# Kernel optimization log

Hardware: AMD Instinct MI355X
Metric: run time of the kernel (lower is better)

The kernel has to match this reference:

```python
import jax, jax.numpy as jnp
import numpy as np

B, T, D_IN = 16, 4096, 512
D_EMB, N_CODES = 256, 1024


def setup_inputs() -> dict:
    key = jax.random.key(0)
    k1, k2, k3, k4 = jax.random.split(key, 4)
    z = jax.random.normal(k1, (B, T, D_IN), dtype=jnp.float32)
    embedding = jax.random.normal(k2, (N_CODES, D_EMB), dtype=jnp.float32)
    # torch Linear weight layout [out_features, in_features], bias=False
    proj_down_w = jax.random.normal(k3, (D_EMB, D_IN), dtype=jnp.float32) * (1.0 / np.sqrt(D_IN))
    proj_up_w = jax.random.normal(k4, (D_IN, D_EMB), dtype=jnp.float32) * (1.0 / np.sqrt(D_EMB))
    return {"z": z, "embedding": embedding, "proj_down_w": proj_down_w, "proj_up_w": proj_up_w}


def _quantize_to_code(z_e, codebook):
    # z_e: [b, t, d]; codebook: [n, d] -> indices [b, t]
    b, t, d = z_e.shape
    z_flat = z_e.reshape(b * t, d)
    dist = (jnp.sum(z_flat * z_flat, axis=1, keepdims=True)
            - 2.0 * (z_flat @ codebook.T)
            + jnp.sum(codebook * codebook, axis=1)[None, :])  # [(b t), n]
    return jnp.argmin(dist, axis=1).reshape(b, t)


def reference(z, embedding, proj_down_w, proj_up_w):
    # proj_down: z @ W_down^T
    z_e = jnp.einsum('btd,ed->bte', z, proj_down_w)  # [b, t, D_EMB]
    code = _quantize_to_code(z_e, embedding)
    z_q = embedding[code]  # gather: [b, t, D_EMB]
    diff2 = (z_q - z_e) ** 2
    commitment_loss = diff2.mean(axis=(1, 2))  # [b]
    codebook_loss = diff2.mean(axis=(1, 2))    # [b] (same values fwd; differ in grad)
    # straight-through estimator (training mode)
    z_q_st = z_e + jax.lax.stop_gradient(z_q - z_e)
    z_q_out = jnp.einsum('bte,de->btd', z_q_st, proj_up_w)  # [b, t, D_IN]
    return (z_q_out, commitment_loss, codebook_loss, code, z_e)
```

## Files before the change

kernel.cpp:

```cpp
#include <hip/hip_runtime.h>
#include <stdint.h>

#define DIN  512
#define DE   256
#define NC   1024
#define M_   65536
#define FLAGCAP 16384

typedef unsigned short u16;
typedef __attribute__((ext_vector_type(8))) short short8_t;
typedef __attribute__((ext_vector_type(4))) float f32x4_t;
typedef __attribute__((ext_vector_type(16))) float f32x16_t;

__device__ __forceinline__ float bf2f(u16 u) {
    unsigned x = ((unsigned)u) << 16; return __builtin_bit_cast(float, x);
}
__device__ __forceinline__ u16 f2bf(float f) {
    unsigned x = __builtin_bit_cast(unsigned, f);
    x += 0x7fffu + ((x >> 16) & 1u);
    return (u16)(x >> 16);
}
__device__ __forceinline__ void cvt8_hl(float4 a, float4 b, short8_t& h, short8_t& l) {
    float v[8] = {a.x,a.y,a.z,a.w, b.x,b.y,b.z,b.w};
#pragma unroll
    for (int j = 0; j < 8; ++j) {
        u16 hh = f2bf(v[j]);
        h[j] = (short)hh; l[j] = (short)f2bf(v[j] - bf2f(hh));
    }
}
__device__ __forceinline__ short8_t cvt8(float4 a, float4 b) {
    float v[8] = {a.x,a.y,a.z,a.w, b.x,b.y,b.z,b.w};
    short8_t h;
#pragma unroll
    for (int j = 0; j < 8; ++j) h[j] = (short)f2bf(v[j]);
    return h;
}

__global__ void k_init(const float* __restrict__ emb, const float* __restrict__ Wd,
                       u16* __restrict__ embH, u16* __restrict__ embL,
                       u16* __restrict__ WdH,  u16* __restrict__ WdL,
                       float* __restrict__ cnorm,
                       float* __restrict__ lossacc, int* __restrict__ flagcnt) {
    int tid = blockIdx.x * 256 + threadIdx.x;
    for (int i = tid; i < DE * DIN; i += 65536) {
        float v = Wd[i]; u16 h = f2bf(v);
        WdH[i] = h; WdL[i] = f2bf(v - bf2f(h));
    }
    for (int i = tid; i < NC * DE; i += 65536) {
        float v = emb[i]; u16 h = f2bf(v);
        embH[i] = h; embL[i] = f2bf(v - bf2f(h));
    }
    if (tid < NC) {
        const float* c = emb + (size_t)tid * DE;
        double s = 0.0;
        for (int j = 0; j < DE; ++j) { double v = c[j]; s += v * v; }
        cnorm[tid] = (float)s;
    }
    if (tid < 16) lossacc[tid] = 0.f;
    if (tid == 16) *flagcnt = 0;
}

__global__ __launch_bounds__(256, 1) void k_pup(
        const float* __restrict__ emb, const float* __restrict__ Wu,
        float* __restrict__ P) {
    __shared__ __align__(16) float le[64][260];
    __shared__ __align__(16) float lw[64][260];
    const int bi = blockIdx.x >> 3, bj = blockIdx.x & 7;
    const int t = threadIdx.x;
    {
        const int r = t >> 2, q = (t & 3) * 64;
        const float* se = emb + (size_t)(bi * 64 + r) * DE + q;
        const float* sw = Wu  + (size_t)(bj * 64 + r) * DE + q;
#pragma unroll
        for (int i = 0; i < 16; ++i) {
            *(float4*)&le[r][q + i * 4] = *(const float4*)(se + i * 4);
            *(float4*)&lw[r][q + i * 4] = *(const float4*)(sw + i * 4);
        }
    }
    __syncthreads();
    const int ci = (t >> 4) * 4, oi = (t & 15) * 4;
    float acc[4][4];
#pragma unroll
    for (int a = 0; a < 4; ++a)
#pragma unroll
        for (int b = 0; b < 4; ++b) acc[a][b] = 0.f;
    for (int k = 0; k < DE; k += 4) {
        float4 av[4], bv[4];
#pragma unroll
        for (int a = 0; a < 4; ++a) av[a] = *(const float4*)&le[ci + a][k];
#pragma unroll
        for (int b = 0; b < 4; ++b) bv[b] = *(const float4*)&lw[oi + b][k];
#pragma unroll
        for (int a = 0; a < 4; ++a)
#pragma unroll
            for (int b = 0; b < 4; ++b)
                acc[a][b] += av[a].x * bv[b].x + av[a].y * bv[b].y
                           + av[a].z * bv[b].z + av[a].w * bv[b].w;
    }
#pragma unroll
    for (int a = 0; a < 4; ++a)
#pragma unroll
        for (int b = 0; b < 4; ++b)
            P[(size_t)(bi * 64 + ci + a) * DIN + bj * 64 + oi + b] = acc[a][b];
}

__global__ __launch_bounds__(256, 2) void k_ze(
        const float* __restrict__ Z,
        const u16* __restrict__ WdH, const u16* __restrict__ WdL,
        float* __restrict__ zeF) {
    __shared__ __align__(16) u16 aH[2][128 * 40];
    __shared__ __align__(16) u16 aL[2][128 * 40];
    const int bz = blockIdx.x >> 1, mh = blockIdx.x & 1;
    const int m0 = bz * 128;
    const int nb = mh * 128;
    const int t = threadIdx.x, lane = t & 63, wv = t >> 6;
    const int lc = lane & 31, hi = lane >> 5;
    const int zsr = t >> 1, zss = (t & 1) * 16;
    const int wdrow = nb + wv * 32 + lc;
    const u16* WdHr = WdH + (size_t)wdrow * DIN;
    const u16* WdLr = WdL + (size_t)wdrow * DIN;

    float4 zf[4];
#define Z_LD(kt_) { \
        const float4* p = (const float4*)(Z + (size_t)(m0 + zsr) * DIN + (kt_) * 32 + zss); \
        zf[0] = p[0]; zf[1] = p[1]; zf[2] = p[2]; zf[3] = p[3]; }
#define Z_WR(b_) { \
        short8_t h0, l0, h1, l1; \
        cvt8_hl(zf[0], zf[1], h0, l0); cvt8_hl(zf[2], zf[3], h1, l1); \
        *(short8_t*)&aH[b_][zsr * 40 + zss]     = h0; \
        *(short8_t*)&aH[b_][zsr * 40 + zss + 8] = h1; \
        *(short8_t*)&aL[b_][zsr * 40 + zss]     = l0; \
        *(short8_t*)&aL[b_][zsr * 40 + zss + 8] = l1; }
#define WD_LD(kt_, H_, L_) { \
        H_[0] = *(const short8_t*)(WdHr + (kt_) * 32 + hi * 8); \
        H_[1] = *(const short8_t*)(WdHr + (kt_) * 32 + 16 + hi * 8); \
        L_[0] = *(const short8_t*)(WdLr + (kt_) * 32 + hi * 8); \
        L_[1] = *(const short8_t*)(WdLr + (kt_) * 32 + 16 + hi * 8); }

    short8_t wh[2], wl[2], nwh[2], nwl[2];
    Z_LD(0);
    WD_LD(0, wh, wl);
    Z_WR(0);
    __syncthreads();

    f32x16_t acc[4];
#pragma unroll
    for (int s = 0; s < 4; ++s)
#pragma unroll
        for (int r = 0; r < 16; ++r) acc[s][r] = 0.f;

    for (int kt = 0; kt < 16; ++kt) {
        if (kt < 15) { Z_LD(kt + 1); WD_LD(kt + 1, nwh, nwl); }
        const int buf = kt & 1;
#pragma unroll
        for (int ks = 0; ks < 2; ++ks) {
#pragma unroll
            for (int s = 0; s < 4; ++s) {
                const int lo = (s * 32 + lc) * 40 + ks * 16 + hi * 8;
                short8_t zh = *(const short8_t*)&aH[buf][lo];
                short8_t zl = *(const short8_t*)&aL[buf][lo];
                acc[s] = __builtin_amdgcn_mfma_f32_32x32x16_bf16(zh, wh[ks], acc[s], 0, 0, 0);
                acc[s] = __builtin_amdgcn_mfma_f32_32x32x16_bf16(zh, wl[ks], acc[s], 0, 0, 0);
                acc[s] = __builtin_amdgcn_mfma_f32_32x32x16_bf16(zl, wh[ks], acc[s], 0, 0, 0);
            }
        }
        if (kt < 15) {
            __syncthreads();
            Z_WR((kt + 1) & 1);
            wh[0] = nwh[0]; wh[1] = nwh[1];
            wl[0] = nwl[0]; wl[1] = nwl[1];
            __syncthreads();
        }
    }
#undef Z_LD
#undef Z_WR
#undef WD_LD

#pragma unroll
    for (int s = 0; s < 4; ++s)
#pragma unroll
        for (int r = 0; r < 16; ++r) {
            const int zr = m0 + s * 32 + (r & 3) + 8 * (r >> 2) + 4 * hi;
            zeF[(size_t)zr * DE + nb + wv * 32 + lc] = acc[s][r];
        }
}

__global__ __launch_bounds__(256, 2) void k_argmin(
        const float* __restrict__ zeF,
        const u16* __restrict__ embH, const u16* __restrict__ embL,
        const float* __restrict__ cnorm,
        u16* __restrict__ codew, float* __restrict__ out_codef,
        int* __restrict__ flaglist,
        int* __restrict__ flagcnt, float* __restrict__ lossacc) {
    __shared__ __align__(16) u16 aH[2][128 * 40];
    __shared__ __align__(16) u16 aL[2][128 * 40];
    __shared__ float lCn[NC];
    __shared__ float lLoss[128];
    const int m0 = blockIdx.x * 128;
    const int t = threadIdx.x, lane = t & 63, wv = t >> 6;
    const int lc = lane & 31, hi = lane >> 5;
    const int zrow = m0 + wv * 32 + lc;

    for (int i = t; i < NC; i += 256) lCn[i] = cnorm[i];

    short8_t bh[16], bl[16];
    float rn = 0.f;
#pragma unroll
    for (int c = 0; c < 16; ++c) {
        const float4* zp = (const float4*)(zeF + (size_t)zrow * DE + c * 16 + hi * 8);
        float4 a = zp[0], b = zp[1];
        rn += a.x*a.x + a.y*a.y + a.z*a.z + a.w*a.w
            + b.x*b.x + b.y*b.y + b.z*b.z + b.w*b.w;
        cvt8_hl(a, b, bh[c], bl[c]);
    }
    rn += __shfl_xor(rn, 32, 64);

#define STAGE_E(ct_, kt_, b_) { \
        _Pragma("unroll") \
        for (int j = 0; j < 2; ++j) { \
            int idx = t + j * 256; \
            int row = idx >> 2, seg = (idx & 3) * 8; \
            size_t off = (size_t)((ct_) * 128 + row) * DE + (kt_) * 32 + seg; \
            uint4 vh = *(const uint4*)(embH + off); \
            uint4 vl = *(const uint4*)(embL + off); \
            *(uint4*)&aH[b_][row * 40 + seg] = vh; \
            *(uint4*)&aL[b_][row * 40 + seg] = vl; \
        } }

    float best = 3.4e38f, sec = 3.4e38f; int bidx = 0;
    STAGE_E(0, 0, 0);
    for (int ct = 0; ct < 8; ++ct) {
        f32x16_t acc[4];
#pragma unroll
        for (int s = 0; s < 4; ++s)
#pragma unroll
            for (int r = 0; r < 16; ++r) acc[s][r] = 0.f;
#pragma unroll
        for (int kt = 0; kt < 8; ++kt) {
            __syncthreads();
            if (kt < 7)      STAGE_E(ct, kt + 1, (kt + 1) & 1)
            else if (ct < 7) STAGE_E(ct + 1, 0, 0)
            const int buf = kt & 1;
#pragma unroll
            for (int ks = 0; ks < 2; ++ks) {
                const int c = kt * 2 + ks;
#pragma unroll
                for (int s = 0; s < 4; ++s) {
                    short8_t ah = *(const short8_t*)&aH[buf][(s * 32 + lc) * 40 + ks * 16 + hi * 8];
                    short8_t al = *(const short8_t*)&aL[buf][(s * 32 + lc) * 40 + ks * 16 + hi * 8];
                    acc[s] = __builtin_amdgcn_mfma_f32_32x32x16_bf16(ah, bh[c], acc[s], 0, 0, 0);
                    acc[s] = __builtin_amdgcn_mfma_f32_32x32x16_bf16(ah, bl[c], acc[s], 0, 0, 0);
                    acc[s] = __builtin_amdgcn_mfma_f32_32x32x16_bf16(al, bh[c], acc[s], 0, 0, 0);
                }
            }
        }
#pragma unroll
        for (int s = 0; s < 4; ++s)
#pragma unroll
            for (int r = 0; r < 16; ++r) {
                const int cidx = ct * 128 + s * 32 + (r & 3) + 8 * (r >> 2) + 4 * hi;
                float d = fmaf(-2.f, acc[s][r], lCn[cidx]);
                bool lt = d < best;
                sec  = lt ? best : fminf(sec, d);
                best = lt ? d : best;
                bidx = lt ? cidx : bidx;
            }
    }
#undef STAGE_E
    {
        float ob = __shfl_xor(best, 32, 64);
        float os = __shfl_xor(sec,  32, 64);
        int   oi = __shfl_xor(bidx, 32, 64);
        float ns = fminf(fminf(sec, os), fmaxf(best, ob));
        if (ob < best) { best = ob; bidx = oi; }
        sec = ns;
    }
    if (lane < 32) {
        codew[zrow] = (u16)bidx;
        out_codef[zrow] = (float)bidx;
        if (sec - best < 0.02f) {
            int pos = atomicAdd(flagcnt, 1);
            if (pos < FLAGCAP) flaglist[pos] = zrow;
        }
        lLoss[wv * 32 + lc] = rn + best;
    }
    __syncthreads();
    for (int str = 64; str > 0; str >>= 1) {
        if (t < str) lLoss[t] += lLoss[t + str];
        __syncthreads();
    }
    if (t == 0) atomicAdd(&lossacc[m0 >> 12], lLoss[0]);
}

__global__ __launch_bounds__(256) void k_refine(
        const float* __restrict__ Z, const float* __restrict__ Wd,
        const float* __restrict__ emb,
        const int* __restrict__ flaglist, const int* __restrict__ flagcnt,
        u16* __restrict__ codew, float* __restrict__ out_codef) {
    __shared__ float  lz[DIN];
    __shared__ double lze[DE];
    __shared__ double ld[256];
    __shared__ int    li[256];
    int n = *flagcnt; if (n < 0) n = 0; if (n > FLAGCAP) n = FLAGCAP;
    int t = threadIdx.x;
    for (int f = blockIdx.x; f < n; f += gridDim.x) {
        int row = flaglist[f] & (M_ - 1);
        __syncthreads();
        for (int i = t; i < DIN; i += 256) lz[i] = Z[(size_t)row * DIN + i];
        __syncthreads();
        double a = 0.0;
        const float* wr = Wd + (size_t)t * DIN;
        for (int k = 0; k < DIN; ++k) a += (double)lz[k] * (double)wr[k];
        lze[t] = a;
        __syncthreads();
        double bd = 1e300; int bi = 0;
        for (int cc = 0; cc < 4; ++cc) {
            int c = cc * 256 + t;
            const float* cr = emb + (size_t)c * DE;
            double s = 0.0;
            for (int e = 0; e < DE; ++e) {
                double diff = lze[e] - (double)cr[e];
                s += diff * diff;
            }
            if (s < bd) { bd = s; bi = c; }
        }
        ld[t] = bd; li[t] = bi;
        __syncthreads();
        for (int str = 128; str > 0; str >>= 1) {
            if (t < str) {
                double od = ld[t + str]; int oi = li[t + str];
                if (od < ld[t] || (od == ld[t] && oi < li[t])) { ld[t] = od; li[t] = oi; }
            }
            __syncthreads();
        }
        if (t == 0) { codew[row] = (u16)li[0]; out_codef[row] = (float)li[0]; }
        __syncthreads();
    }
}

__global__ void k_loss(const float* __restrict__ lossacc,
                       float* __restrict__ out_commit, float* __restrict__ out_codebook) {
    int tid = threadIdx.x;
    if (tid < 16) {
        float v = lossacc[tid] * (1.f / 1048576.f);
        out_commit[tid] = v; out_codebook[tid] = v;
    }
}

__global__ __launch_bounds__(256) void k_gather(
        const float* __restrict__ P, const float* __restrict__ out_code,
        float* __restrict__ out) {
    const int g = blockIdx.x * 256 + threadIdx.x;
    const float4* P4 = (const float4*)P;
    float4* O4 = (float4*)out;
    for (int u = g; u < M_ * 128; u += 524288) {
        const int row = u >> 7, seg = u & 127;
        const int c = (int)out_code[row] & (NC - 1);
        O4[(size_t)row * 128 + seg] = P4[(size_t)c * 128 + seg];
    }
}

__global__ __launch_bounds__(512) void k_gemm3(
        const float* __restrict__ emb, const float* __restrict__ Wu,
        const float* __restrict__ out_code, float* __restrict__ out) {
    __shared__ __align__(16) u16 gA[128 * 264];
    const int bz = blockIdx.x >> 1, nh = blockIdx.x & 1;
    const int m0 = bz * 128;
    const int t = threadIdx.x, lane = t & 63, wv = t >> 6;
    const int lr = lane & 15, lg = lane >> 4;
    {
        const int row = t >> 2, seg = (t & 3) * 64;
        const int code = (int)out_code[m0 + row] & (NC - 1);
        const float* src = emb + (size_t)code * DE + seg;
#pragma unroll
        for (int j = 0; j < 8; ++j) {
            const float4* p = (const float4*)(src + j * 8);
            *(short8_t*)&gA[row * 264 + seg + j * 8] = cvt8(p[0], p[1]);
        }
    }
    __syncthreads();

    const int nbase = nh * 256 + wv * 32;
    f32x4_t acc[8][2];
#pragma unroll
    for (int i = 0; i < 8; ++i)
#pragma unroll
        for (int j = 0; j < 2; ++j) acc[i][j] = (f32x4_t){0.f, 0.f, 0.f, 0.f};

#pragma unroll
    for (int kt = 0; kt < 8; ++kt) {
        const int k0 = kt * 32 + lg * 8;
        short8_t b0, b1;
        {
            const float4* p = (const float4*)(Wu + (size_t)(nbase + lr) * DE + k0);
            b0 = cvt8(p[0], p[1]);
            const float4* q = (const float4*)(Wu + (size_t)(nbase + 16 + lr) * DE + k0);
            b1 = cvt8(q[0], q[1]);
        }
#pragma unroll
        for (int mi = 0; mi < 8; ++mi) {
            short8_t a = *(const short8_t*)&gA[(mi * 16 + lr) * 264 + k0];
            acc[mi][0] = __builtin_amdgcn_mfma_f32_16x16x32_bf16(a, b0, acc[mi][0], 0, 0, 0);
            acc[mi][1] = __builtin_amdgcn_mfma_f32_16x16x32_bf16(a, b1, acc[mi][1], 0, 0, 0);
        }
    }
#pragma unroll
    for (int mi = 0; mi < 8; ++mi)
#pragma unroll
        for (int reg = 0; reg < 4; ++reg) {
            const int zr = m0 + mi * 16 + lg * 4 + reg;
            out[(size_t)zr * DIN + nbase + lr]      = acc[mi][0][reg];
            out[(size_t)zr * DIN + nbase + 16 + lr] = acc[mi][1][reg];
        }
}

extern "C" void kernel_launch(void* const* d_in, const int* in_sizes, int n_in,
                              void* d_out, int out_size, void* d_ws, size_t ws_size,
                              hipStream_t stream) {
    const float* Z   = (const float*)d_in[0];
    const float* E   = (const float*)d_in[1];
    const float* Wd  = (const float*)d_in[2];
    const float* Wu  = (const float*)d_in[3];

    float* out       = (float*)d_out;
    float* out_zq    = out;
    float* out_com   = out + 33554432;
    float* out_cb    = out + 33554448;
    float* out_code  = out + 33554464;
    float* out_ze    = out + 33620000;

    char* scr = (char*)d_out;
    u16*   embH     = (u16*)  (scr + 0);
    u16*   embL     = (u16*)  (scr + 524288);
    u16*   WdH      = (u16*)  (scr + 1048576);
    u16*   WdL      = (u16*)  (scr + 1310720);
    float* cnorm    = (float*)(scr + 1572864);
    u16*   codew    = (u16*)  (scr + 1839104);
    int*   flaglist = (int*)  (scr + 1970176);
    int*   flagcnt  = (int*)  (scr + 2035712);
    float* lossacc  = (float*)(scr + 2035776);
    (void)in_sizes; (void)n_in; (void)out_size;

    const bool useP = (ws_size >= (size_t)NC * DIN * sizeof(float));
    float* P = (float*)d_ws;

    k_init  <<<256,  256, 0, stream>>>(E, Wd, embH, embL, WdH, WdL, cnorm,
                                       lossacc, flagcnt);
    if (useP)
        k_pup <<<128, 256, 0, stream>>>(E, Wu, P);
    k_ze    <<<1024, 256, 0, stream>>>(Z, WdH, WdL, out_ze);
    k_argmin<<<512,  256, 0, stream>>>(out_ze, embH, embL, cnorm,
                                       codew, out_code, flaglist, flagcnt, lossacc);
    k_refine<<<128,  256, 0, stream>>>(Z, Wd, E, flaglist, flagcnt, codew, out_code);
    k_loss  <<<1,    64,  0, stream>>>(lossacc, out_com, out_cb);
    if (useP)
        k_gather<<<2048, 256, 0, stream>>>(P, out_code, out_zq);
    else
        k_gemm3 <<<1024, 512, 0, stream>>>(E, Wu, out_code, out_zq);
}
```

Measured before the change: 350.8 us.

## Process two row groups per wave in argmin to reuse staged codebook tiles

Each argmin block now handles 256 z_e rows instead of 128, with every wave keeping two 32-row B fragments and two accumulator sets. Each codebook tile staged in LDS then feeds twice as many MFMAs, which halves codebook global loads and LDS reads per row. The costs are much higher register pressure (launch bounds drop to one block per SM), only 256 blocks across the CUs, and less latency hiding. The lossacc index m0>>12 still lines up with batch boundaries because 4096 is a multiple of 256.

```diff
diff --git a/kernel.cpp b/kernel.cpp
--- a/kernel.cpp
+++ b/kernel.cpp
@@ -185,7 +185,7 @@
         }
 }
 
-__global__ __launch_bounds__(256, 2) void k_argmin(
+__global__ __launch_bounds__(256, 1) void k_argmin(
         const float* __restrict__ zeF,
         const u16* __restrict__ embH, const u16* __restrict__ embL,
         const float* __restrict__ cnorm,
@@ -195,25 +195,35 @@
     __shared__ __align__(16) u16 aH[2][128 * 40];
     __shared__ __align__(16) u16 aL[2][128 * 40];
     __shared__ float lCn[NC];
-    __shared__ float lLoss[128];
-    const int m0 = blockIdx.x * 128;
+    __shared__ float lLoss[256];
+    const int m0 = blockIdx.x * 256;
     const int t = threadIdx.x, lane = t & 63, wv = t >> 6;
     const int lc = lane & 31, hi = lane >> 5;
-    const int zrow = m0 + wv * 32 + lc;
+    const int r0 = m0 + wv * 64 + lc;
+    const int r1 = r0 + 32;
 
     for (int i = t; i < NC; i += 256) lCn[i] = cnorm[i];
 
-    short8_t bh[16], bl[16];
-    float rn = 0.f;
+    short8_t b0h[16], b0l[16], b1h[16], b1l[16];
+    float rn0 = 0.f, rn1 = 0.f;
 #pragma unroll
     for (int c = 0; c < 16; ++c) {
-        const float4* zp = (const float4*)(zeF + (size_t)zrow * DE + c * 16 + hi * 8);
+        const float4* zp = (const float4*)(zeF + (size_t)r0 * DE + c * 16 + hi * 8);
         float4 a = zp[0], b = zp[1];
-        rn += a.x*a.x + a.y*a.y + a.z*a.z + a.w*a.w
-            + b.x*b.x + b.y*b.y + b.z*b.z + b.w*b.w;
-        cvt8_hl(a, b, bh[c], bl[c]);
-    }
-    rn += __shfl_xor(rn, 32, 64);
+        rn0 += a.x*a.x + a.y*a.y + a.z*a.z + a.w*a.w
+             + b.x*b.x + b.y*b.y + b.z*b.z + b.w*b.w;
+        cvt8_hl(a, b, b0h[c], b0l[c]);
+    }
+#pragma unroll
+    for (int c = 0; c < 16; ++c) {
+        const float4* zp = (const float4*)(zeF + (size_t)r1 * DE + c * 16 + hi * 8);
+        float4 a = zp[0], b = zp[1];
+        rn1 += a.x*a.x + a.y*a.y + a.z*a.z + a.w*a.w
+             + b.x*b.x + b.y*b.y + b.z*b.z + b.w*b.w;
+        cvt8_hl(a, b, b1h[c], b1l[c]);
+    }
+    rn0 += __shfl_xor(rn0, 32, 64);
+    rn1 += __shfl_xor(rn1, 32, 64);
 
 #define STAGE_E(ct_, kt_, b_) { \
         _Pragma("unroll") \
@@ -227,14 +237,15 @@
             *(uint4*)&aL[b_][row * 40 + seg] = vl; \
         } }
 
-    float best = 3.4e38f, sec = 3.4e38f; int bidx = 0;
+    float best0 = 3.4e38f, sec0 = 3.4e38f; int bidx0 = 0;
+    float best1 = 3.4e38f, sec1 = 3.4e38f; int bidx1 = 0;
     STAGE_E(0, 0, 0);
     for (int ct = 0; ct < 8; ++ct) {
-        f32x16_t acc[4];
+        f32x16_t acc0[4], acc1[4];
 #pragma unroll
         for (int s = 0; s < 4; ++s)
 #pragma unroll
-            for (int r = 0; r < 16; ++r) acc[s][r] = 0.f;
+            for (int r = 0; r < 16; ++r) { acc0[s][r] = 0.f; acc1[s][r] = 0.f; }
 #pragma unroll
         for (int kt = 0; kt < 8; ++kt) {
             __syncthreads();
@@ -248,9 +259,12 @@
                 for (int s = 0; s < 4; ++s) {
                     short8_t ah = *(const short8_t*)&aH[buf][(s * 32 + lc) * 40 + ks * 16 + hi * 8];
                     short8_t al = *(const short8_t*)&aL[buf][(s * 32 + lc) * 40 + ks * 16 + hi * 8];
-                    acc[s] = __builtin_amdgcn_mfma_f32_32x32x16_bf16(ah, bh[c], acc[s], 0, 0, 0);
-                    acc[s] = __builtin_amdgcn_mfma_f32_32x32x16_bf16(ah, bl[c], acc[s], 0, 0, 0);
-                    acc[s] = __builtin_amdgcn_mfma_f32_32x32x16_bf16(al, bh[c], acc[s], 0, 0, 0);
+                    acc0[s] = __builtin_amdgcn_mfma_f32_32x32x16_bf16(ah, b0h[c], acc0[s], 0, 0, 0);
+                    acc0[s] = __builtin_amdgcn_mfma_f32_32x32x16_bf16(ah, b0l[c], acc0[s], 0, 0, 0);
+                    acc0[s] = __builtin_amdgcn_mfma_f32_32x32x16_bf16(al, b0h[c], acc0[s], 0, 0, 0);
+                    acc1[s] = __builtin_amdgcn_mfma_f32_32x32x16_bf16(ah, b1h[c], acc1[s], 0, 0, 0);
+                    acc1[s] = __builtin_amdgcn_mfma_f32_32x32x16_bf16(ah, b1l[c], acc1[s], 0, 0, 0);
+                    acc1[s] = __builtin_amdgcn_mfma_f32_32x32x16_bf16(al, b1h[c], acc1[s], 0, 0, 0);
                 }
             }
         }
@@ -259,33 +273,54 @@
 #pragma unroll
             for (int r = 0; r < 16; ++r) {
                 const int cidx = ct * 128 + s * 32 + (r & 3) + 8 * (r >> 2) + 4 * hi;
-                float d = fmaf(-2.f, acc[s][r], lCn[cidx]);
-                bool lt = d < best;
-                sec  = lt ? best : fminf(sec, d);
-                best = lt ? d : best;
-                bidx = lt ? cidx : bidx;
+                const float cn = lCn[cidx];
+                float d0 = fmaf(-2.f, acc0[s][r], cn);
+                bool lt0 = d0 < best0;
+                sec0  = lt0 ? best0 : fminf(sec0, d0);
+                best0 = lt0 ? d0 : best0;
+                bidx0 = lt0 ? cidx : bidx0;
+                float d1 = fmaf(-2.f, acc1[s][r], cn);
+                bool lt1 = d1 < best1;
+                sec1  = lt1 ? best1 : fminf(sec1, d1);
+                best1 = lt1 ? d1 : best1;
+                bidx1 = lt1 ? cidx : bidx1;
             }
     }
 #undef STAGE_E
     {
-        float ob = __shfl_xor(best, 32, 64);
-        float os = __shfl_xor(sec,  32, 64);
-        int   oi = __shfl_xor(bidx, 32, 64);
-        float ns = fminf(fminf(sec, os), fmaxf(best, ob));
-        if (ob < best) { best = ob; bidx = oi; }
-        sec = ns;
+        float ob = __shfl_xor(best0, 32, 64);
+        float os = __shfl_xor(sec0,  32, 64);
+        int   oi = __shfl_xor(bidx0, 32, 64);
+        float ns = fminf(fminf(sec0, os), fmaxf(best0, ob));
+        if (ob < best0) { best0 = ob; bidx0 = oi; }
+        sec0 = ns;
+    }
+    {
+        float ob = __shfl_xor(best1, 32, 64);
+        float os = __shfl_xor(sec1,  32, 64);
+        int   oi = __shfl_xor(bidx1, 32, 64);
+        float ns = fminf(fminf(sec1, os), fmaxf(best1, ob));
+        if (ob < best1) { best1 = ob; bidx1 = oi; }
+        sec1 = ns;
     }
     if (lane < 32) {
-        codew[zrow] = (u16)bidx;
-        out_codef[zrow] = (float)bidx;
-        if (sec - best < 0.02f) {
+        codew[r0] = (u16)bidx0;
+        out_codef[r0] = (float)bidx0;
+        codew[r1] = (u16)bidx1;
+        out_codef[r1] = (float)bidx1;
+        if (sec0 - best0 < 0.02f) {
             int pos = atomicAdd(flagcnt, 1);
-            if (pos < FLAGCAP) flaglist[pos] = zrow;
-        }
-        lLoss[wv * 32 + lc] = rn + best;
+            if (pos < FLAGCAP) flaglist[pos] = r0;
+        }
+        if (sec1 - best1 < 0.02f) {
+            int pos = atomicAdd(flagcnt, 1);
+            if (pos < FLAGCAP) flaglist[pos] = r1;
+        }
+        lLoss[wv * 64 + lc]      = rn0 + best0;
+        lLoss[wv * 64 + 32 + lc] = rn1 + best1;
     }
     __syncthreads();
-    for (int str = 64; str > 0; str >>= 1) {
+    for (int str = 128; str > 0; str >>= 1) {
         if (t < str) lLoss[t] += lLoss[t + str];
         __syncthreads();
     }
@@ -449,7 +484,7 @@
     if (useP)
         k_pup <<<128, 256, 0, stream>>>(E, Wu, P);
     k_ze    <<<1024, 256, 0, stream>>>(Z, WdH, WdL, out_ze);
-    k_argmin<<<512,  256, 0, stream>>>(out_ze, embH, embL, cnorm,
+    k_argmin<<<256,  256, 0, stream>>>(out_ze, embH, embL, cnorm,
                                        codew, out_code, flaglist, flagcnt, lossacc);
     k_refine<<<128,  256, 0, stream>>>(Z, Wd, E, flaglist, flagcnt, codew, out_code);
     k_loss  <<<1,    64,  0, stream>>>(lossacc, out_com, out_cb);
```

After: 375.7 us. 7.1% more time.
